# Performance work log

Hardware: AMD Instinct MI355X
Metric: run time of the kernel (lower is better)

The kernel has to match this reference:

```python
import jax, jax.numpy as jnp
import numpy as np


def _sobel_kernels(dtype):
    # Faithful to the torch code: each kernel has shape (1,3,3) in (kd,kh,kw),
    # i.e. a 2D Sobel applied slice-wise, but conv3d uses padding=1 on ALL dims
    # so the output depth is D+2.
    sx = np.array([[[-1, 0, 1], [-2, 0, 2], [-1, 0, 1]]], dtype=np.float32)  # (1,3,3)
    sy = np.transpose(sx, (0, 2, 1))                                          # transpose(1,2)
    sz = np.array([[[-1, -2, -1], [0, 0, 0], [1, 2, 1]]], dtype=np.float32)
    k = np.stack([sx, sy, sz])[:, None]  # (3 out, 1 in, 1, 3, 3)
    return jnp.asarray(k, dtype)


def setup_inputs() -> dict:
    key = jax.random.key(0)
    k1, k2 = jax.random.split(key)
    B, C, D, H, W = 2, 4, 96, 160, 160
    pred = jax.random.normal(k1, (B, C, D, H, W), dtype=jnp.float32)
    target = jax.random.randint(k2, (B, D, H, W), 0, C)
    return {"pred": pred, "target": target}


def reference(pred, target):
    B, C, D, H, W = pred.shape
    p = jax.nn.softmax(pred, axis=1)                                   # (B,C,D,H,W)
    t = jax.nn.one_hot(target, C, dtype=pred.dtype)                    # (B,D,H,W,C)
    t = jnp.transpose(t, (0, 4, 1, 2, 3))                              # (B,C,D,H,W)
    k = _sobel_kernels(pred.dtype)

    def sobel(x):
        # fold class into batch; 3 output channels = x/y/z gradients
        x = x.reshape(B * C, 1, D, H, W)
        return jax.lax.conv_general_dilated(
            x, k, window_strides=(1, 1, 1), padding=[(1, 1)] * 3,
            dimension_numbers=("NCDHW", "OIDHW", "NCDHW"))           # (B*C,3,D+2,H+2,W+2)

    diff = sobel(p) - sobel(t)
    # Each torch mse_loss averages over a (B,1,D+2,H+2,W+2) tensor; the 3*C
    # means are summed, then divided by num_classes.
    per_tensor = B * (D + 2) * (H + 2) * (W + 2)
    loss = jnp.sum(diff * diff) / per_tensor / C
    return loss
```

## Files before the change

kernel.cpp:

```cpp
#include <hip/hip_runtime.h>
#include <hip/hip_fp16.h>

#define NB 2
#define NC 4
#define ND 96
#define NH 160
#define NW 160

constexpr int TH    = 8;
constexpr int SR    = TH + 2;
constexpr int NBAND = NH / TH;
constexpr int NSLOT = SR * NW / 4;
constexpr int PCELL = SR * NW;
constexpr int ZCELL = PCELL;
constexpr int NPART = NBAND * NB * ND;
constexpr float SCALE = 1.0f / (2.0f * 98.0f * 162.0f * 162.0f * 4.0f);

__device__ __forceinline__ __half2 ld_h2(const unsigned int* p, int i) {
    return __builtin_bit_cast(__half2, p[i]);
}

__device__ __forceinline__ void qcalc(float p0, float p1, float p2, float p3,
                                      int t, bool valid,
                                      unsigned int& ha, unsigned int& hb) {
    float q0 = 0.f, q1 = 0.f, q2 = 0.f, q3 = 0.f;
    if (valid) {
        const float m  = fmaxf(fmaxf(p0, p1), fmaxf(p2, p3));
        const float e0 = __expf(p0 - m);
        const float e1 = __expf(p1 - m);
        const float e2 = __expf(p2 - m);
        const float e3 = __expf(p3 - m);
        const float inv = 1.0f / (e0 + e1 + e2 + e3);
        q0 = e0 * inv - (t == 0 ? 1.f : 0.f);
        q1 = e1 * inv - (t == 1 ? 1.f : 0.f);
        q2 = e2 * inv - (t == 2 ? 1.f : 0.f);
        q3 = e3 * inv - (t == 3 ? 1.f : 0.f);
    }
    ha = __builtin_bit_cast(unsigned int, __floats2half2_rn(q0, q1));
    hb = __builtin_bit_cast(unsigned int, __floats2half2_rn(q2, q3));
}

__global__ __launch_bounds__(256) void boundary_loss_kernel(
    const float* __restrict__ pred,
    const int*   __restrict__ target,
    float* __restrict__ part)
{
    __shared__ unsigned int pa[PCELL + 4];
    __shared__ unsigned int pb[PCELL + 4];
    __shared__ float wsum[4];

    const int tid   = threadIdx.x;
    const int slice = blockIdx.y;
    const int b     = slice / ND;
    const int d     = slice - b * ND;
    const int y0    = blockIdx.x * TH;

    const size_t cs4   = (size_t)ND * NH * NW / 4;
    const size_t pbase = ((size_t)b * NC * ND + d) * (size_t)(NH * NW);
    const size_t tbase = ((size_t)b * ND + d) * (size_t)(NH * NW);

    const int  rA   = tid / 40;
    const int  cA   = tid - rA * 40;
    const int  gyA  = y0 - 1 + rA;
    const bool vA   = (gyA >= 0) && (gyA < NH);
    const int  gyAc = min(max(gyA, 0), NH - 1);

    const int  sB   = tid + 256;
    const bool hasB = (sB < NSLOT);
    const int  rB   = sB / 40;
    const int  cB   = sB - rB * 40;
    const int  gyB  = y0 - 1 + rB;
    const bool vB   = hasB && (gyB >= 0) && (gyB < NH);
    const int  gyBc = min(max(gyB, 0), NH - 1);

    const float4* ppA = (const float4*)(pred + pbase + (size_t)gyAc * NW) + cA;
    const float4 a0 = ppA[0];
    const float4 a1 = ppA[cs4];
    const float4 a2 = ppA[2 * cs4];
    const float4 a3 = ppA[3 * cs4];
    const int4   ta = ((const int4*)(target + tbase + (size_t)gyAc * NW))[cA];

    const int cBs  = hasB ? cB : 0;
    const int gyBs = hasB ? gyBc : 0;
    const float4* ppB = (const float4*)(pred + pbase + (size_t)gyBs * NW) + cBs;
    const float4 b0 = ppB[0];
    const float4 b1 = ppB[cs4];
    const float4 b2 = ppB[2 * cs4];
    const float4 b3 = ppB[3 * cs4];
    const int4   tb = ((const int4*)(target + tbase + (size_t)gyBs * NW))[cBs];

    {
        uint4 wa, wb;
        qcalc(a0.x, a1.x, a2.x, a3.x, ta.x, vA, wa.x, wb.x);
        qcalc(a0.y, a1.y, a2.y, a3.y, ta.y, vA, wa.y, wb.y);
        qcalc(a0.z, a1.z, a2.z, a3.z, ta.z, vA, wa.z, wb.z);
        qcalc(a0.w, a1.w, a2.w, a3.w, ta.w, vA, wa.w, wb.w);
        ((uint4*)pa)[rA * 40 + cA] = wa;
        ((uint4*)pb)[rA * 40 + cA] = wb;
    }
    if (hasB) {
        uint4 wa, wb;
        qcalc(b0.x, b1.x, b2.x, b3.x, tb.x, vB, wa.x, wb.x);
        qcalc(b0.y, b1.y, b2.y, b3.y, tb.y, vB, wa.y, wb.y);
        qcalc(b0.z, b1.z, b2.z, b3.z, tb.z, vB, wa.z, wb.z);
        qcalc(b0.w, b1.w, b2.w, b3.w, tb.w, vB, wa.w, wb.w);
        ((uint4*)pa)[rB * 40 + cB] = wa;
        ((uint4*)pb)[rB * 40 + cB] = wb;
    }
    if (tid == 0) { pa[ZCELL] = 0u; pb[ZCELL] = 0u; }
    __syncthreads();

    float acc = 0.f;
    if (tid < NW) {
        int am = tid;
        int al = (tid > 0)      ? tid - 1 : ZCELL;
        int ar = (tid < NW - 1) ? tid + 1 : ZCELL;
        const int il = (tid > 0)      ? NW : 0;
        const int ir = (tid < NW - 1) ? NW : 0;

        const __half2 two = __floats2half2_rn(2.f, 2.f);
        const __half2 hz  = __floats2half2_rn(0.f, 0.f);
        __half2 smmA = hz, smA = hz, dmmA = hz, dmA = hz;
        __half2 smmB = hz, smB = hz, dmmB = hz, dmB = hz;

#define CLS(P, smm, sm, dmm, dm)                                          \
        do {                                                              \
            const __half2 l = ld_h2(P, al);                               \
            const __half2 m = ld_h2(P, am);                               \
            const __half2 r = ld_h2(P, ar);                               \
            const __half2 sn = __hadd2(__hfma2(m, two, l), r);            \
            const __half2 dn = __hsub2(r, l);                             \
            if (t >= 2) {                                                 \
                const __half2 gx = __hadd2(__hfma2(dm, two, dmm), dn);    \
                const __half2 gy = __hsub2(sn, smm);                      \
                const __half2 rs = __hfma2(__hmul2(gy, gy), two,          \
                                           __hmul2(gx, gx));              \
                acc += __low2float(rs) + __high2float(rs);                \
            }                                                             \
            smm = sm; sm = sn; dmm = dm; dm = dn;                         \
        } while (0)

        #pragma unroll
        for (int t = 0; t < SR; ++t) {
            CLS(pa, smmA, smA, dmmA, dmA);
            CLS(pb, smmB, smB, dmmB, dmB);
            am += NW; al += il; ar += ir;
        }
#undef CLS
    }

    #pragma unroll
    for (int off = 32; off > 0; off >>= 1)
        acc += __shfl_down(acc, off, 64);
    if ((tid & 63) == 0) wsum[tid >> 6] = acc;
    __syncthreads();
    if (tid == 0) {
        part[blockIdx.y * NBAND + blockIdx.x] =
            wsum[0] + wsum[1] + wsum[2] + wsum[3];
    }
}

__global__ __launch_bounds__(256) void reduce_partials_kernel(
    const float* __restrict__ part, float* __restrict__ out)
{
    const int tid = threadIdx.x;
    float s = 0.f;
    #pragma unroll
    for (int i = 0; i < NPART / 256; ++i)
        s += part[tid + i * 256];
    #pragma unroll
    for (int off = 32; off > 0; off >>= 1)
        s += __shfl_down(s, off, 64);
    __shared__ float wsum[4];
    if ((tid & 63) == 0) wsum[tid >> 6] = s;
    __syncthreads();
    if (tid == 0)
        out[0] = (wsum[0] + wsum[1] + wsum[2] + wsum[3]) * SCALE;
}

extern "C" void kernel_launch(void* const* d_in, const int* in_sizes, int n_in,
                              void* d_out, int out_size, void* d_ws, size_t ws_size,
                              hipStream_t stream) {
    const float* pred   = (const float*)d_in[0];
    const int*   target = (const int*)d_in[1];
    float*       out    = (float*)d_out;
    float*       part   = (float*)d_ws;

    dim3 grid(NBAND, NB * ND);
    boundary_loss_kernel<<<grid, 256, 0, stream>>>(pred, target, part);
    reduce_partials_kernel<<<1, 256, 0, stream>>>(part, out);
}
```

Measured before the change: 128.1 us.

## Process several row bands per block with double-buffered LDS prefetch

Each block now handles five consecutive 8-row bands instead of one. It prefetches the next band's pred and target values into registers while computing the Sobel terms on the current band, using two LDS buffers that alternate. This is meant to hide global-load latency and cut the per-block launch overhead. In exchange it uses more registers and twice the LDS, which may lower occupancy, and it launches fewer blocks. NPART drops from 3840 to 768, which is still a multiple of 256, so the reduce kernel stays valid.

```diff
diff --git a/kernel.cpp b/kernel.cpp
--- a/kernel.cpp
+++ b/kernel.cpp
@@ -10,10 +10,12 @@
 constexpr int TH    = 8;
 constexpr int SR    = TH + 2;
 constexpr int NBAND = NH / TH;
+constexpr int M     = 5;
+constexpr int SEG   = NBAND / M;
 constexpr int NSLOT = SR * NW / 4;
 constexpr int PCELL = SR * NW;
 constexpr int ZCELL = PCELL;
-constexpr int NPART = NBAND * NB * ND;
+constexpr int NPART = NB * ND * SEG;
 constexpr float SCALE = 1.0f / (2.0f * 98.0f * 162.0f * 162.0f * 4.0f);
 
 __device__ __forceinline__ __half2 ld_h2(const unsigned int* p, int i) {
@@ -40,20 +42,25 @@
     hb = __builtin_bit_cast(unsigned int, __floats2half2_rn(q2, q3));
 }
 
+struct Regs {
+    float4 a0, a1, a2, a3; int4 ta; bool vA;
+    float4 b0, b1, b2, b3; int4 tb; bool vB;
+};
+
 __global__ __launch_bounds__(256) void boundary_loss_kernel(
     const float* __restrict__ pred,
     const int*   __restrict__ target,
     float* __restrict__ part)
 {
-    __shared__ unsigned int pa[PCELL + 4];
-    __shared__ unsigned int pb[PCELL + 4];
+    __shared__ unsigned int pa[2][PCELL + 4];
+    __shared__ unsigned int pb[2][PCELL + 4];
     __shared__ float wsum[4];
 
     const int tid   = threadIdx.x;
     const int slice = blockIdx.y;
     const int b     = slice / ND;
     const int d     = slice - b * ND;
-    const int y0    = blockIdx.x * TH;
+    const int yseg  = blockIdx.x * (M * TH);
 
     const size_t cs4   = (size_t)ND * NH * NW / 4;
     const size_t pbase = ((size_t)b * NC * ND + d) * (size_t)(NH * NW);
@@ -61,92 +68,106 @@
 
     const int  rA   = tid / 40;
     const int  cA   = tid - rA * 40;
-    const int  gyA  = y0 - 1 + rA;
-    const bool vA   = (gyA >= 0) && (gyA < NH);
-    const int  gyAc = min(max(gyA, 0), NH - 1);
-
     const int  sB   = tid + 256;
     const bool hasB = (sB < NSLOT);
     const int  rB   = sB / 40;
     const int  cB   = sB - rB * 40;
-    const int  gyB  = y0 - 1 + rB;
-    const bool vB   = hasB && (gyB >= 0) && (gyB < NH);
-    const int  gyBc = min(max(gyB, 0), NH - 1);
-
-    const float4* ppA = (const float4*)(pred + pbase + (size_t)gyAc * NW) + cA;
-    const float4 a0 = ppA[0];
-    const float4 a1 = ppA[cs4];
-    const float4 a2 = ppA[2 * cs4];
-    const float4 a3 = ppA[3 * cs4];
-    const int4   ta = ((const int4*)(target + tbase + (size_t)gyAc * NW))[cA];
-
-    const int cBs  = hasB ? cB : 0;
-    const int gyBs = hasB ? gyBc : 0;
-    const float4* ppB = (const float4*)(pred + pbase + (size_t)gyBs * NW) + cBs;
-    const float4 b0 = ppB[0];
-    const float4 b1 = ppB[cs4];
-    const float4 b2 = ppB[2 * cs4];
-    const float4 b3 = ppB[3 * cs4];
-    const int4   tb = ((const int4*)(target + tbase + (size_t)gyBs * NW))[cBs];
-
-    {
+    const int  cBs  = hasB ? cB : 0;
+
+    auto load_band = [&](int y0) {
+        Regs r;
+        const int gyA  = y0 - 1 + rA;
+        r.vA = (gyA >= 0) && (gyA < NH);
+        const int gyAc = min(max(gyA, 0), NH - 1);
+        const float4* ppA = (const float4*)(pred + pbase + (size_t)gyAc * NW) + cA;
+        r.a0 = ppA[0]; r.a1 = ppA[cs4]; r.a2 = ppA[2 * cs4]; r.a3 = ppA[3 * cs4];
+        r.ta = ((const int4*)(target + tbase + (size_t)gyAc * NW))[cA];
+
+        const int gyB  = y0 - 1 + rB;
+        r.vB = hasB && (gyB >= 0) && (gyB < NH);
+        const int gyBc = hasB ? min(max(gyB, 0), NH - 1) : 0;
+        const float4* ppB = (const float4*)(pred + pbase + (size_t)gyBc * NW) + cBs;
+        r.b0 = ppB[0]; r.b1 = ppB[cs4]; r.b2 = ppB[2 * cs4]; r.b3 = ppB[3 * cs4];
+        r.tb = ((const int4*)(target + tbase + (size_t)gyBc * NW))[cBs];
+        return r;
+    };
+
+    auto stage_band = [&](const Regs& r, unsigned int* Pa, unsigned int* Pb) {
         uint4 wa, wb;
-        qcalc(a0.x, a1.x, a2.x, a3.x, ta.x, vA, wa.x, wb.x);
-        qcalc(a0.y, a1.y, a2.y, a3.y, ta.y, vA, wa.y, wb.y);
-        qcalc(a0.z, a1.z, a2.z, a3.z, ta.z, vA, wa.z, wb.z);
-        qcalc(a0.w, a1.w, a2.w, a3.w, ta.w, vA, wa.w, wb.w);
-        ((uint4*)pa)[rA * 40 + cA] = wa;
-        ((uint4*)pb)[rA * 40 + cA] = wb;
-    }
-    if (hasB) {
-        uint4 wa, wb;
-        qcalc(b0.x, b1.x, b2.x, b3.x, tb.x, vB, wa.x, wb.x);
-        qcalc(b0.y, b1.y, b2.y, b3.y, tb.y, vB, wa.y, wb.y);
-        qcalc(b0.z, b1.z, b2.z, b3.z, tb.z, vB, wa.z, wb.z);
-        qcalc(b0.w, b1.w, b2.w, b3.w, tb.w, vB, wa.w, wb.w);
-        ((uint4*)pa)[rB * 40 + cB] = wa;
-        ((uint4*)pb)[rB * 40 + cB] = wb;
-    }
-    if (tid == 0) { pa[ZCELL] = 0u; pb[ZCELL] = 0u; }
+        qcalc(r.a0.x, r.a1.x, r.a2.x, r.a3.x, r.ta.x, r.vA, wa.x, wb.x);
+        qcalc(r.a0.y, r.a1.y, r.a2.y, r.a3.y, r.ta.y, r.vA, wa.y, wb.y);
+        qcalc(r.a0.z, r.a1.z, r.a2.z, r.a3.z, r.ta.z, r.vA, wa.z, wb.z);
+        qcalc(r.a0.w, r.a1.w, r.a2.w, r.a3.w, r.ta.w, r.vA, wa.w, wb.w);
+        ((uint4*)Pa)[rA * 40 + cA] = wa;
+        ((uint4*)Pb)[rA * 40 + cA] = wb;
+        if (hasB) {
+            qcalc(r.b0.x, r.b1.x, r.b2.x, r.b3.x, r.tb.x, r.vB, wa.x, wb.x);
+            qcalc(r.b0.y, r.b1.y, r.b2.y, r.b3.y, r.tb.y, r.vB, wa.y, wb.y);
+            qcalc(r.b0.z, r.b1.z, r.b2.z, r.b3.z, r.tb.z, r.vB, wa.z, wb.z);
+            qcalc(r.b0.w, r.b1.w, r.b2.w, r.b3.w, r.tb.w, r.vB, wa.w, wb.w);
+            ((uint4*)Pa)[rB * 40 + cB] = wa;
+            ((uint4*)Pb)[rB * 40 + cB] = wb;
+        }
+    };
+
+    auto compute_band = [&](const unsigned int* Pa, const unsigned int* Pb) {
+        float a = 0.f;
+        if (tid < NW) {
+            int am = tid;
+            int al = (tid > 0)      ? tid - 1 : ZCELL;
+            int ar = (tid < NW - 1) ? tid + 1 : ZCELL;
+            const int il = (tid > 0)      ? NW : 0;
+            const int ir = (tid < NW - 1) ? NW : 0;
+
+            const __half2 two = __floats2half2_rn(2.f, 2.f);
+            const __half2 hz  = __floats2half2_rn(0.f, 0.f);
+            __half2 smmA = hz, smA = hz, dmmA = hz, dmA = hz;
+            __half2 smmB = hz, smB = hz, dmmB = hz, dmB = hz;
+
+#define CLS(P, smm, sm, dmm, dm)                                          \
+            do {                                                          \
+                const __half2 l = ld_h2(P, al);                           \
+                const __half2 m = ld_h2(P, am);                           \
+                const __half2 r = ld_h2(P, ar);                           \
+                const __half2 sn = __hadd2(__hfma2(m, two, l), r);        \
+                const __half2 dn = __hsub2(r, l);                         \
+                if (t >= 2) {                                             \
+                    const __half2 gx = __hadd2(__hfma2(dm, two, dmm), dn);\
+                    const __half2 gy = __hsub2(sn, smm);                  \
+                    const __half2 rs = __hfma2(__hmul2(gy, gy), two,      \
+                                               __hmul2(gx, gx));          \
+                    a += __low2float(rs) + __high2float(rs);              \
+                }                                                         \
+                smm = sm; sm = sn; dmm = dm; dm = dn;                     \
+            } while (0)
+
+            #pragma unroll
+            for (int t = 0; t < SR; ++t) {
+                CLS(Pa, smmA, smA, dmmA, dmA);
+                CLS(Pb, smmB, smB, dmmB, dmB);
+                am += NW; al += il; ar += ir;
+            }
+#undef CLS
+        }
+        return a;
+    };
+
+    if (tid == 0) {
+        pa[0][ZCELL] = 0u; pb[0][ZCELL] = 0u;
+        pa[1][ZCELL] = 0u; pb[1][ZCELL] = 0u;
+    }
+    Regs r0 = load_band(yseg);
+    stage_band(r0, pa[0], pb[0]);
     __syncthreads();
 
     float acc = 0.f;
-    if (tid < NW) {
-        int am = tid;
-        int al = (tid > 0)      ? tid - 1 : ZCELL;
-        int ar = (tid < NW - 1) ? tid + 1 : ZCELL;
-        const int il = (tid > 0)      ? NW : 0;
-        const int ir = (tid < NW - 1) ? NW : 0;
-
-        const __half2 two = __floats2half2_rn(2.f, 2.f);
-        const __half2 hz  = __floats2half2_rn(0.f, 0.f);
-        __half2 smmA = hz, smA = hz, dmmA = hz, dmA = hz;
-        __half2 smmB = hz, smB = hz, dmmB = hz, dmB = hz;
-
-#define CLS(P, smm, sm, dmm, dm)                                          \
-        do {                                                              \
-            const __half2 l = ld_h2(P, al);                               \
-            const __half2 m = ld_h2(P, am);                               \
-            const __half2 r = ld_h2(P, ar);                               \
-            const __half2 sn = __hadd2(__hfma2(m, two, l), r);            \
-            const __half2 dn = __hsub2(r, l);                             \
-            if (t >= 2) {                                                 \
-                const __half2 gx = __hadd2(__hfma2(dm, two, dmm), dn);    \
-                const __half2 gy = __hsub2(sn, smm);                      \
-                const __half2 rs = __hfma2(__hmul2(gy, gy), two,          \
-                                           __hmul2(gx, gx));              \
-                acc += __low2float(rs) + __high2float(rs);                \
-            }                                                             \
-            smm = sm; sm = sn; dmm = dm; dm = dn;                         \
-        } while (0)
-
-        #pragma unroll
-        for (int t = 0; t < SR; ++t) {
-            CLS(pa, smmA, smA, dmmA, dmA);
-            CLS(pb, smmB, smB, dmmB, dmB);
-            am += NW; al += il; ar += ir;
-        }
-#undef CLS
+    #pragma unroll
+    for (int i = 0; i < M; ++i) {
+        Regs rn;
+        if (i + 1 < M) rn = load_band(yseg + (i + 1) * TH);
+        acc += compute_band(pa[i & 1], pb[i & 1]);
+        if (i + 1 < M) stage_band(rn, pa[(i + 1) & 1], pb[(i + 1) & 1]);
+        __syncthreads();
     }
 
     #pragma unroll
@@ -155,7 +176,7 @@
     if ((tid & 63) == 0) wsum[tid >> 6] = acc;
     __syncthreads();
     if (tid == 0) {
-        part[blockIdx.y * NBAND + blockIdx.x] =
+        part[blockIdx.y * SEG + blockIdx.x] =
             wsum[0] + wsum[1] + wsum[2] + wsum[3];
     }
 }
@@ -186,7 +207,7 @@
     float*       out    = (float*)d_out;
     float*       part   = (float*)d_ws;
 
-    dim3 grid(NBAND, NB * ND);
+    dim3 grid(SEG, NB * ND);
     boundary_loss_kernel<<<grid, 256, 0, stream>>>(pred, target, part);
     reduce_partials_kernel<<<1, 256, 0, stream>>>(part, out);
 }
```

After: 129.4 us. About the same (+1.0%).
